# Performance work log

Measured on AMD Instinct MI355X. Metric: run time of the kernel, lower is better.

The kernel has to match this reference:

```python
import jax, jax.numpy as jnp
import numpy as np

LEAK = 0.5  # LeakyReLU negative slope


def _binarize(w):
    # sign binarization with straight-through estimator (standard BinarizeConv2d /
    # CIM-sim quantized-weight behavior): forward uses sign(w) in {-1,+1},
    # backward passes gradient straight through.
    wb = jnp.where(w >= 0, 1.0, -1.0).astype(w.dtype)
    return w + jax.lax.stop_gradient(wb - w)


def _conv(x, w, b):
    # NCHW / OIHW, stride 1, no padding (matches nn.Conv2d(k, stride=1) defaults)
    y = jax.lax.conv_general_dilated(
        x, _binarize(w), window_strides=(1, 1), padding='VALID',
        dimension_numbers=('NCHW', 'OIHW', 'NCHW'))
    return y + b[None, :, None, None]


def _leaky(x):
    return jnp.where(x >= 0, x, LEAK * x)


def _maxpool2(x):
    # MaxPool2d(kernel_size=2), stride 2, floor mode == VALID reduce_window
    return jax.lax.reduce_window(x, -jnp.inf, jax.lax.max,
                                 (1, 1, 2, 2), (1, 1, 2, 2), 'VALID')


def setup_inputs() -> dict:
    key = jax.random.key(0)
    ks = jax.random.split(key, 9)
    f32 = jnp.float32
    return {
        'x':  jax.random.normal(ks[0], (32, 1, 224, 224), f32),
        'w1': jax.random.normal(ks[1], (128, 1, 3, 3), f32) * 0.1,
        'b1': jax.random.normal(ks[2], (128,), f32) * 0.1,
        'w2': jax.random.normal(ks[3], (64, 128, 3, 3), f32) * 0.1,
        'b2': jax.random.normal(ks[4], (64,), f32) * 0.1,
        'w3': jax.random.normal(ks[5], (32, 64, 3, 3), f32) * 0.1,
        'b3': jax.random.normal(ks[6], (32,), f32) * 0.1,
        'w4': jax.random.normal(ks[7], (8, 32, 3, 2), f32) * 0.1,
        'b4': jax.random.normal(ks[8], (8,), f32) * 0.1,
    }


def reference(x, w1, b1, w2, b2, w3, b3, w4, b4):
    x = _maxpool2(_leaky(_conv(x, w1, b1)))   # [B,128,111,111]
    x = _maxpool2(_leaky(_conv(x, w2, b2)))   # [B,64,54,54]
    x = _maxpool2(_leaky(_conv(x, w3, b3)))   # [B,32,26,26]
    x = _conv(x, w4, b4)                       # [B,8,24,25]
    return x.reshape(x.shape[0], -1)           # [B,4800]
```

## Files before the change

### kernel.cpp

```cpp
#include <hip/hip_runtime.h>
#include <hip/hip_bf16.h>

using bf16 = __hip_bfloat16;
typedef short  short8  __attribute__((ext_vector_type(8)));
typedef float  f32x4   __attribute__((ext_vector_type(4)));
typedef float  f32x16  __attribute__((ext_vector_type(16)));
typedef unsigned short us4 __attribute__((ext_vector_type(4)));

static __device__ __forceinline__ bf16  f2b(float v) { return __float2bfloat16(v); }
static __device__ __forceinline__ unsigned short f2bu(float v) {
    bf16 t = __float2bfloat16(v);
    return *(unsigned short*)&t;
}

__device__ __forceinline__ void pack32_one(const float* __restrict__ w,
                                           bf16* __restrict__ o, int i, int IC) {
    int j = i & 7;
    int l = (i >> 3) & 63;
    int f = i >> 9;
    int ICD16 = IC >> 4;
    int cc = f % ICD16;
    int t  = f / ICD16;
    int r  = t % 9;
    int mt = t / 9;
    int oc = mt * 32 + (l & 31);
    int ic = cc * 16 + ((l >> 5) << 3) + j;
    o[i] = f2b((w[(oc * IC + ic) * 9 + r] >= 0.f) ? 1.f : -1.f);
}

__global__ __launch_bounds__(256) void binpack_kernel(
    const float* __restrict__ w1, const float* __restrict__ w2,
    const float* __restrict__ w3, const float* __restrict__ w4,
    bf16* __restrict__ w1m, bf16* __restrict__ wA2,
    bf16* __restrict__ wA3, float* __restrict__ wc4) {
    int i = blockIdx.x * 256 + threadIdx.x;
    if (i < 73728) {
        pack32_one(w2, wA2, i, 128);
    } else if (i < 73728 + 18432) {
        pack32_one(w3, wA3, i - 73728, 64);
    } else if (i < 73728 + 18432 + 2048) {
        int k = i - (73728 + 18432);
        int j = k & 7, l = (k >> 3) & 63, mt = k >> 9;
        int ch = mt * 32 + (l & 31);
        int t = ((l >> 5) << 3) + j;
        w1m[k] = f2b(t < 9 ? ((w1[ch * 9 + t] >= 0.f) ? 1.f : -1.f) : 0.f);
    } else if (i < 73728 + 18432 + 2048 + 1536) {
        int k = i - (73728 + 18432 + 2048);
        int oc = k / 192, rem = k % 192;
        int ic = rem / 6, r = rem % 6;
        wc4[oc * 192 + r * 32 + ic] = (w4[k] >= 0.f) ? 1.f : -1.f;
    }
}

__global__ __launch_bounds__(256, 4) void conv1_kernel(
    const float* __restrict__ x, const bf16* __restrict__ w1m,
    const float* __restrict__ b1, bf16* __restrict__ a1) {
    __shared__ float xt[10][20];
    const int tid = threadIdx.x;
    const int b = blockIdx.z;
    const int pw0 = blockIdx.x * 8;
    const int ph0 = blockIdx.y * 4;
    const int r0 = ph0 * 2;
    const int c0 = pw0 * 2;

    if (tid < 180) {
        int row = tid / 18, col = tid - row * 18;
        int gr = r0 + row, gc = c0 + col;
        xt[row][col] = (gr < 224 && gc < 224)
                           ? x[((size_t)b * 224 + gr) * 224 + gc] : 0.f;
    }
    __syncthreads();

    const int w  = tid >> 6;
    const int l  = tid & 63;
    const int lc = l & 15;
    const int r2 = (l >> 4) & 1;
    const int hh = l >> 5;

    short8 af[4];
#pragma unroll
    for (int mt = 0; mt < 4; ++mt)
        af[mt] = ((const short8*)w1m)[mt * 64 + l];

    const int hl = 2 * w + r2;
    short8 bf;
    if (hh == 0) {
        bf[0] = (short)f2bu(xt[hl + 0][lc + 0]);
        bf[1] = (short)f2bu(xt[hl + 0][lc + 1]);
        bf[2] = (short)f2bu(xt[hl + 0][lc + 2]);
        bf[3] = (short)f2bu(xt[hl + 1][lc + 0]);
        bf[4] = (short)f2bu(xt[hl + 1][lc + 1]);
        bf[5] = (short)f2bu(xt[hl + 1][lc + 2]);
        bf[6] = (short)f2bu(xt[hl + 2][lc + 0]);
        bf[7] = (short)f2bu(xt[hl + 2][lc + 1]);
    } else {
        bf[0] = (short)f2bu(xt[hl + 2][lc + 2]);
        bf[1] = 0; bf[2] = 0; bf[3] = 0;
        bf[4] = 0; bf[5] = 0; bf[6] = 0; bf[7] = 0;
    }

    f32x16 acc[4];
#pragma unroll
    for (int mt = 0; mt < 4; ++mt) {
#pragma unroll
        for (int q = 0; q < 16; ++q) acc[mt][q] = 0.f;
        acc[mt] = __builtin_amdgcn_mfma_f32_32x32x16_bf16(af[mt], bf, acc[mt],
                                                          0, 0, 0);
    }

    const bool wr = ((l & 17) == 0);
    const int pw = pw0 + (lc >> 1);
    const int ph = ph0 + w;
    if (ph < 111 && pw < 111) {
#pragma unroll
        for (int mt = 0; mt < 4; ++mt) {
#pragma unroll
            for (int g = 0; g < 4; ++g) {
                f32x4 bias = *(const f32x4*)(b1 + mt * 32 + 8 * g + 4 * hh);
                us4 o;
#pragma unroll
                for (int q2 = 0; q2 < 4; ++q2) {
                    float v = acc[mt][g * 4 + q2] + bias[q2];
                    v = (v >= 0.f) ? v : 0.5f * v;
                    float m1 = fmaxf(v, __shfl_xor(v, 1));
                    float m  = fmaxf(m1, __shfl_xor(m1, 16));
                    o[q2] = f2bu(m);
                }
                if (wr)
                    *(us4*)(&a1[((size_t)(b * 111 + ph) * 111 + pw) * 128 +
                                mt * 32 + 8 * g + 4 * hh]) = o;
            }
        }
    }
}

template <int IC, int OC, int IN, int POOL>
__global__ __launch_bounds__(256, 2) void convmfma_kernel(
    const bf16* __restrict__ in, const bf16* __restrict__ wAp,
    const float* __restrict__ bias, bf16* __restrict__ out) {
    constexpr int MT = OC / 32;
    constexpr int CHUNKS = IC / 32;
    constexpr int ICD16 = IC / 16;
    constexpr int WROW = 10, WCOL = 34;
    __shared__ __align__(16) char smem[WROW * WCOL * 64];

    const int tid = threadIdx.x;
    const int b = blockIdx.z;
    const int oh0 = blockIdx.y * 8;
    const int ow0 = blockIdx.x * 32;

    const int w  = tid >> 6;
    const int l  = tid & 63;
    const int n  = l & 31;
    const int hh = l >> 5;

    f32x16 acc[MT][2];
#pragma unroll
    for (int mt = 0; mt < MT; ++mt)
#pragma unroll
        for (int nt = 0; nt < 2; ++nt)
#pragma unroll
            for (int q = 0; q < 16; ++q) acc[mt][nt][q] = 0.f;

    for (int chunk = 0; chunk < CHUNKS; ++chunk) {
        if (chunk) __syncthreads();
        {
            const bf16* src = in + (size_t)b * IN * IN * IC + chunk * 32;
            for (int u = tid; u < WROW * WCOL * 4; u += 256) {
                int slot = u & 3, cell = u >> 2;
                int row = cell / WCOL, col = cell - row * WCOL;
                int gr = oh0 + row, gc = ow0 + col;
                f32x4 v = {0.f, 0.f, 0.f, 0.f};
                if (gr < IN && gc < IN)
                    v = *(const f32x4*)(src + ((size_t)gr * IN + gc) * IC + slot * 8);
                *(f32x4*)(smem + cell * 64 + ((slot ^ ((col >> 1) & 3)) << 4)) = v;
            }
        }
        __syncthreads();

#pragma unroll
        for (int cc = 0; cc < 2; ++cc) {
#pragma unroll
            for (int kw = 0; kw < 3; ++kw) {
                const int wincol = n + kw;
                const int sx = (wincol >> 1) & 3;
                const int slot = cc * 2 + hh;
                short8 brow[4];
#pragma unroll
                for (int ar = 0; ar < 4; ++ar) {
                    int cell = (2 * w + ar) * WCOL + wincol;
                    brow[ar] = *(const short8*)(
                        smem + cell * 64 + ((slot ^ sx) << 4));
                }
#pragma unroll
                for (int kh = 0; kh < 3; ++kh) {
                    const int r = kh * 3 + kw;
                    short8 af[MT];
#pragma unroll
                    for (int mt = 0; mt < MT; ++mt)
                        af[mt] = ((const short8*)wAp)[
                            (((mt * 9 + r) * ICD16) + chunk * 2 + cc) * 64 + l];
#pragma unroll
                    for (int nt = 0; nt < 2; ++nt)
#pragma unroll
                        for (int mt = 0; mt < MT; ++mt)
                            acc[mt][nt] = __builtin_amdgcn_mfma_f32_32x32x16_bf16(
                                af[mt], brow[nt + kh], acc[mt][nt], 0, 0, 0);
                }
            }
        }
    }

    const int pw = blockIdx.x * 16 + (n >> 1);
    const int ph = blockIdx.y * 4 + w;
    const bool wr = ((l & 1) == 0) && ph < POOL && pw < POOL;
#pragma unroll
    for (int mt = 0; mt < MT; ++mt) {
#pragma unroll
        for (int g = 0; g < 4; ++g) {
            f32x4 bs = *(const f32x4*)(bias + mt * 32 + 8 * g + 4 * hh);
            us4 o;
#pragma unroll
            for (int q2 = 0; q2 < 4; ++q2) {
                int q = g * 4 + q2;
                float v = fmaxf(acc[mt][0][q], acc[mt][1][q]);
                v = fmaxf(v, __shfl_xor(v, 1));
                v += bs[q2];
                v = (v >= 0.f) ? v : 0.5f * v;
                o[q2] = f2bu(v);
            }
            if (wr)
                *(us4*)(&out[((size_t)(b * POOL + ph) * POOL + pw) * OC +
                             mt * 32 + 8 * g + 4 * hh]) = o;
        }
    }
}

__global__ __launch_bounds__(256) void conv4_kernel(
    const bf16* __restrict__ a3, const float* __restrict__ wc4,
    const float* __restrict__ b4, float* __restrict__ out) {
    int i = blockIdx.x * 256 + threadIdx.x;
    if (i >= 32 * 4800) return;
    int b = i / 4800;
    int rem = i % 4800;
    int oc = rem / 600;
    int r2 = rem % 600;
    int oh = r2 / 25, ow = r2 % 25;

    float acc = b4[oc];
    int rr = 0;
#pragma unroll
    for (int kh = 0; kh < 3; ++kh) {
#pragma unroll
        for (int kw = 0; kw < 2; ++kw, ++rr) {
            const bf16* xp = a3 + ((size_t)(b * 26 + oh + kh) * 26 + (ow + kw)) * 32;
            const float* wp = wc4 + oc * 192 + rr * 32;
            short8 x0 = *(const short8*)(xp);
            short8 x1 = *(const short8*)(xp + 8);
            short8 x2 = *(const short8*)(xp + 16);
            short8 x3 = *(const short8*)(xp + 24);
#pragma unroll
            for (int j = 0; j < 8; ++j) {
                union { short s; unsigned short u; } u0{x0[j]}, u1{x1[j]}, u2{x2[j]}, u3{x3[j]};
                acc += wp[j]      * __bfloat162float(__hip_bfloat16_raw{u0.u});
                acc += wp[8 + j]  * __bfloat162float(__hip_bfloat16_raw{u1.u});
                acc += wp[16 + j] * __bfloat162float(__hip_bfloat16_raw{u2.u});
                acc += wp[24 + j] * __bfloat162float(__hip_bfloat16_raw{u3.u});
            }
        }
    }
    out[i] = acc;
}

extern "C" void kernel_launch(void* const* d_in, const int* in_sizes, int n_in,
                              void* d_out, int out_size, void* d_ws, size_t ws_size,
                              hipStream_t stream) {
    const float* x  = (const float*)d_in[0];
    const float* w1 = (const float*)d_in[1];
    const float* b1 = (const float*)d_in[2];
    const float* w2 = (const float*)d_in[3];
    const float* b2 = (const float*)d_in[4];
    const float* w3 = (const float*)d_in[5];
    const float* b3 = (const float*)d_in[6];
    const float* w4 = (const float*)d_in[7];
    const float* b4 = (const float*)d_in[8];
    float* out = (float*)d_out;

    char* ws = (char*)d_ws;
    size_t off = 0;
    auto alloc = [&](size_t bytes) {
        void* p = ws + off;
        off = (off + bytes + 255) & ~(size_t)255;
        return p;
    };
    bf16* a1 = (bf16*)alloc((size_t)32 * 111 * 111 * 128 * 2);
    bf16* a2 = (bf16*)alloc((size_t)32 * 54 * 54 * 64 * 2);
    bf16* a3 = (bf16*)alloc((size_t)32 * 26 * 26 * 32 * 2);
    bf16* w1m = (bf16*)alloc(2048 * 2);
    bf16* wAp2 = (bf16*)alloc(73728 * 2);
    bf16* wAp3 = (bf16*)alloc(18432 * 2);
    float* wc4 = (float*)alloc(1536 * 4);

    binpack_kernel<<<dim3((95744 + 255) / 256), 256, 0, stream>>>(
        w1, w2, w3, w4, w1m, wAp2, wAp3, wc4);

    dim3 g1(14, 28, 32);
    conv1_kernel<<<g1, 256, 0, stream>>>(x, w1m, b1, a1);

    dim3 g2(4, 14, 32);
    convmfma_kernel<128, 64, 111, 54><<<g2, 256, 0, stream>>>(a1, wAp2, b2, a2);

    dim3 g3(2, 7, 32);
    convmfma_kernel<64, 32, 54, 26><<<g3, 256, 0, stream>>>(a2, wAp3, b3, a3);

    conv4_kernel<<<dim3((32 * 4800 + 255) / 256), 256, 0, stream>>>(
        a3, wc4, b4, out);
}
```

Baseline: 258.0 us.

## Enlarge conv tiles: wider conv1 tile, taller conv2/conv3 tiles with more register accumulators

Conv1 now has each wave cover 32 output columns with two MFMA N-tiles, so the pool pairs are combined inside a lane pair and the cross-half shuffle goes away. Conv2 and conv3 tiles grow to 16 output rows per block: each wave holds 4 N-tiles of accumulators, and the weight fragments for all three kh are loaded once per kw and reused across those tiles. The LDS swizzle gains an extra XOR term to cut bank conflicts. The larger tiles reduce halo reloads and weight traffic, but they raise register and LDS pressure and leave fewer blocks to fill the GPU.

```diff
diff --git a/kernel.cpp b/kernel.cpp
--- a/kernel.cpp
+++ b/kernel.cpp
@@ -52,19 +52,19 @@
     }
 }
 
-__global__ __launch_bounds__(256, 4) void conv1_kernel(
+__global__ __launch_bounds__(256, 2) void conv1_kernel(
     const float* __restrict__ x, const bf16* __restrict__ w1m,
     const float* __restrict__ b1, bf16* __restrict__ a1) {
-    __shared__ float xt[10][20];
+    __shared__ float xt[10][34];
     const int tid = threadIdx.x;
     const int b = blockIdx.z;
-    const int pw0 = blockIdx.x * 8;
+    const int pw0 = blockIdx.x * 16;
     const int ph0 = blockIdx.y * 4;
     const int r0 = ph0 * 2;
     const int c0 = pw0 * 2;
 
-    if (tid < 180) {
-        int row = tid / 18, col = tid - row * 18;
+    for (int u = tid; u < 10 * 34; u += 256) {
+        int row = u / 34, col = u - row * 34;
         int gr = r0 + row, gc = c0 + col;
         xt[row][col] = (gr < 224 && gc < 224)
                            ? x[((size_t)b * 224 + gr) * 224 + gc] : 0.f;
@@ -73,8 +73,7 @@
 
     const int w  = tid >> 6;
     const int l  = tid & 63;
-    const int lc = l & 15;
-    const int r2 = (l >> 4) & 1;
+    const int n  = l & 31;
     const int hh = l >> 5;
 
     short8 af[4];
@@ -82,54 +81,60 @@
     for (int mt = 0; mt < 4; ++mt)
         af[mt] = ((const short8*)w1m)[mt * 64 + l];
 
-    const int hl = 2 * w + r2;
-    short8 bf;
-    if (hh == 0) {
-        bf[0] = (short)f2bu(xt[hl + 0][lc + 0]);
-        bf[1] = (short)f2bu(xt[hl + 0][lc + 1]);
-        bf[2] = (short)f2bu(xt[hl + 0][lc + 2]);
-        bf[3] = (short)f2bu(xt[hl + 1][lc + 0]);
-        bf[4] = (short)f2bu(xt[hl + 1][lc + 1]);
-        bf[5] = (short)f2bu(xt[hl + 1][lc + 2]);
-        bf[6] = (short)f2bu(xt[hl + 2][lc + 0]);
-        bf[7] = (short)f2bu(xt[hl + 2][lc + 1]);
-    } else {
-        bf[0] = (short)f2bu(xt[hl + 2][lc + 2]);
-        bf[1] = 0; bf[2] = 0; bf[3] = 0;
-        bf[4] = 0; bf[5] = 0; bf[6] = 0; bf[7] = 0;
-    }
-
-    f32x16 acc[4];
+    short8 bfr[2];
+#pragma unroll
+    for (int nt = 0; nt < 2; ++nt) {
+        const int hl = 2 * w + nt;
+        short8 bf;
+        if (hh == 0) {
+            bf[0] = (short)f2bu(xt[hl + 0][n + 0]);
+            bf[1] = (short)f2bu(xt[hl + 0][n + 1]);
+            bf[2] = (short)f2bu(xt[hl + 0][n + 2]);
+            bf[3] = (short)f2bu(xt[hl + 1][n + 0]);
+            bf[4] = (short)f2bu(xt[hl + 1][n + 1]);
+            bf[5] = (short)f2bu(xt[hl + 1][n + 2]);
+            bf[6] = (short)f2bu(xt[hl + 2][n + 0]);
+            bf[7] = (short)f2bu(xt[hl + 2][n + 1]);
+        } else {
+            bf[0] = (short)f2bu(xt[hl + 2][n + 2]);
+            bf[1] = 0; bf[2] = 0; bf[3] = 0;
+            bf[4] = 0; bf[5] = 0; bf[6] = 0; bf[7] = 0;
+        }
+        bfr[nt] = bf;
+    }
+
+    f32x16 acc[4][2];
+#pragma unroll
+    for (int mt = 0; mt < 4; ++mt)
+#pragma unroll
+        for (int nt = 0; nt < 2; ++nt) {
+#pragma unroll
+            for (int q = 0; q < 16; ++q) acc[mt][nt][q] = 0.f;
+            acc[mt][nt] = __builtin_amdgcn_mfma_f32_32x32x16_bf16(
+                af[mt], bfr[nt], acc[mt][nt], 0, 0, 0);
+        }
+
+    const int pw = pw0 + (n >> 1);
+    const int ph = ph0 + w;
+    const bool wr = ((l & 1) == 0) && ph < 111 && pw < 111;
 #pragma unroll
     for (int mt = 0; mt < 4; ++mt) {
 #pragma unroll
-        for (int q = 0; q < 16; ++q) acc[mt][q] = 0.f;
-        acc[mt] = __builtin_amdgcn_mfma_f32_32x32x16_bf16(af[mt], bf, acc[mt],
-                                                          0, 0, 0);
-    }
-
-    const bool wr = ((l & 17) == 0);
-    const int pw = pw0 + (lc >> 1);
-    const int ph = ph0 + w;
-    if (ph < 111 && pw < 111) {
-#pragma unroll
-        for (int mt = 0; mt < 4; ++mt) {
-#pragma unroll
-            for (int g = 0; g < 4; ++g) {
-                f32x4 bias = *(const f32x4*)(b1 + mt * 32 + 8 * g + 4 * hh);
-                us4 o;
-#pragma unroll
-                for (int q2 = 0; q2 < 4; ++q2) {
-                    float v = acc[mt][g * 4 + q2] + bias[q2];
-                    v = (v >= 0.f) ? v : 0.5f * v;
-                    float m1 = fmaxf(v, __shfl_xor(v, 1));
-                    float m  = fmaxf(m1, __shfl_xor(m1, 16));
-                    o[q2] = f2bu(m);
-                }
-                if (wr)
-                    *(us4*)(&a1[((size_t)(b * 111 + ph) * 111 + pw) * 128 +
-                                mt * 32 + 8 * g + 4 * hh]) = o;
-            }
+        for (int g = 0; g < 4; ++g) {
+            f32x4 bs = *(const f32x4*)(b1 + mt * 32 + 8 * g + 4 * hh);
+            us4 o;
+#pragma unroll
+            for (int q2 = 0; q2 < 4; ++q2) {
+                int q = g * 4 + q2;
+                float v = fmaxf(acc[mt][0][q], acc[mt][1][q]);
+                v = fmaxf(v, __shfl_xor(v, 1));
+                v += bs[q2];
+                v = fmaxf(v, 0.5f * v);
+                o[q2] = f2bu(v);
+            }
+            if (wr)
+                *(us4*)(&a1[((size_t)(b * 111 + ph) * 111 + pw) * 128 +
+                            mt * 32 + 8 * g + 4 * hh]) = o;
         }
     }
 }
@@ -141,12 +146,12 @@
     constexpr int MT = OC / 32;
     constexpr int CHUNKS = IC / 32;
     constexpr int ICD16 = IC / 16;
-    constexpr int WROW = 10, WCOL = 34;
+    constexpr int WROW = 18, WCOL = 34;
     __shared__ __align__(16) char smem[WROW * WCOL * 64];
 
     const int tid = threadIdx.x;
     const int b = blockIdx.z;
-    const int oh0 = blockIdx.y * 8;
+    const int oh0 = blockIdx.y * 16;
     const int ow0 = blockIdx.x * 32;
 
     const int w  = tid >> 6;
@@ -154,11 +159,11 @@
     const int n  = l & 31;
     const int hh = l >> 5;
 
-    f32x16 acc[MT][2];
+    f32x16 acc[MT][4];
 #pragma unroll
     for (int mt = 0; mt < MT; ++mt)
 #pragma unroll
-        for (int nt = 0; nt < 2; ++nt)
+        for (int nt = 0; nt < 4; ++nt)
 #pragma unroll
             for (int q = 0; q < 16; ++q) acc[mt][nt][q] = 0.f;
 
@@ -173,7 +178,8 @@
                 f32x4 v = {0.f, 0.f, 0.f, 0.f};
                 if (gr < IN && gc < IN)
                     v = *(const f32x4*)(src + ((size_t)gr * IN + gc) * IC + slot * 8);
-                *(f32x4*)(smem + cell * 64 + ((slot ^ ((col >> 1) & 3)) << 4)) = v;
+                int sx = ((col >> 1) ^ (col >> 3)) & 3;
+                *(f32x4*)(smem + cell * 64 + ((slot ^ sx) << 4)) = v;
             }
         }
         __syncthreads();
@@ -182,56 +188,60 @@
         for (int cc = 0; cc < 2; ++cc) {
 #pragma unroll
             for (int kw = 0; kw < 3; ++kw) {
-                const int wincol = n + kw;
-                const int sx = (wincol >> 1) & 3;
+                short8 af[MT][3];
+#pragma unroll
+                for (int mt = 0; mt < MT; ++mt)
+#pragma unroll
+                    for (int kh = 0; kh < 3; ++kh)
+                        af[mt][kh] = ((const short8*)wAp)[
+                            (((mt * 9 + kh * 3 + kw) * ICD16) +
+                             chunk * 2 + cc) * 64 + l];
+                const int col = n + kw;
+                const int sx = ((col >> 1) ^ (col >> 3)) & 3;
                 const int slot = cc * 2 + hh;
-                short8 brow[4];
-#pragma unroll
-                for (int ar = 0; ar < 4; ++ar) {
-                    int cell = (2 * w + ar) * WCOL + wincol;
+                short8 brow[6];
+#pragma unroll
+                for (int ar = 0; ar < 6; ++ar) {
+                    int cell = (4 * w + ar) * WCOL + col;
                     brow[ar] = *(const short8*)(
                         smem + cell * 64 + ((slot ^ sx) << 4));
                 }
 #pragma unroll
-                for (int kh = 0; kh < 3; ++kh) {
-                    const int r = kh * 3 + kw;
-                    short8 af[MT];
-#pragma unroll
-                    for (int mt = 0; mt < MT; ++mt)
-                        af[mt] = ((const short8*)wAp)[
-                            (((mt * 9 + r) * ICD16) + chunk * 2 + cc) * 64 + l];
-#pragma unroll
-                    for (int nt = 0; nt < 2; ++nt)
+                for (int kh = 0; kh < 3; ++kh)
+#pragma unroll
+                    for (int nt = 0; nt < 4; ++nt)
 #pragma unroll
                         for (int mt = 0; mt < MT; ++mt)
                             acc[mt][nt] = __builtin_amdgcn_mfma_f32_32x32x16_bf16(
-                                af[mt], brow[nt + kh], acc[mt][nt], 0, 0, 0);
+                                af[mt][kh], brow[nt + kh], acc[mt][nt], 0, 0, 0);
+            }
+        }
+    }
+
+    const int pw = blockIdx.x * 16 + (n >> 1);
+#pragma unroll
+    for (int ntp = 0; ntp < 2; ++ntp) {
+        const int ph = blockIdx.y * 8 + 2 * w + ntp;
+        const bool wr = ((l & 1) == 0) && ph < POOL && pw < POOL;
+#pragma unroll
+        for (int mt = 0; mt < MT; ++mt) {
+#pragma unroll
+            for (int g = 0; g < 4; ++g) {
+                f32x4 bs = *(const f32x4*)(bias + mt * 32 + 8 * g + 4 * hh);
+                us4 o;
+#pragma unroll
+                for (int q2 = 0; q2 < 4; ++q2) {
+                    int q = g * 4 + q2;
+                    float v = fmaxf(acc[mt][2 * ntp][q], acc[mt][2 * ntp + 1][q]);
+                    v = fmaxf(v, __shfl_xor(v, 1));
+                    v += bs[q2];
+                    v = fmaxf(v, 0.5f * v);
+                    o[q2] = f2bu(v);
                 }
-            }
-        }
-    }
-
-    const int pw = blockIdx.x * 16 + (n >> 1);
-    const int ph = blockIdx.y * 4 + w;
-    const bool wr = ((l & 1) == 0) && ph < POOL && pw < POOL;
-#pragma unroll
-    for (int mt = 0; mt < MT; ++mt) {
-#pragma unroll
-        for (int g = 0; g < 4; ++g) {
-            f32x4 bs = *(const f32x4*)(bias + mt * 32 + 8 * g + 4 * hh);
-            us4 o;
-#pragma unroll
-            for (int q2 = 0; q2 < 4; ++q2) {
-                int q = g * 4 + q2;
-                float v = fmaxf(acc[mt][0][q], acc[mt][1][q]);
-                v = fmaxf(v, __shfl_xor(v, 1));
-                v += bs[q2];
-                v = (v >= 0.f) ? v : 0.5f * v;
-                o[q2] = f2bu(v);
-            }
-            if (wr)
-                *(us4*)(&out[((size_t)(b * POOL + ph) * POOL + pw) * OC +
-                             mt * 32 + 8 * g + 4 * hh]) = o;
+                if (wr)
+                    *(us4*)(&out[((size_t)(b * POOL + ph) * POOL + pw) * OC +
+                                 mt * 32 + 8 * g + 4 * hh]) = o;
+            }
         }
     }
 }
@@ -304,13 +314,13 @@
     binpack_kernel<<<dim3((95744 + 255) / 256), 256, 0, stream>>>(
         w1, w2, w3, w4, w1m, wAp2, wAp3, wc4);
 
-    dim3 g1(14, 28, 32);
+    dim3 g1(7, 28, 32);
     conv1_kernel<<<g1, 256, 0, stream>>>(x, w1m, b1, a1);
 
-    dim3 g2(4, 14, 32);
+    dim3 g2(4, 7, 32);
     convmfma_kernel<128, 64, 111, 54><<<g2, 256, 0, stream>>>(a1, wAp2, b2, a2);
 
-    dim3 g3(2, 7, 32);
+    dim3 g3(2, 4, 32);
     convmfma_kernel<64, 32, 54, 26><<<g3, 256, 0, stream>>>(a2, wAp3, b3, a3);
 
     conv4_kernel<<<dim3((32 * 4800 + 255) / 256), 256, 0, stream>>>(
```

Result: faster. 238.1 us (-7.7%).
